# Kernel tuning notes

Hardware: AMD Instinct MI355X
Metric: run time of the kernel (lower is better)

The kernel has to match this reference:

```python
import jax, jax.numpy as jnp
import numpy as np


def setup_inputs() -> dict:
    key = jax.random.key(0)
    k1, k2, k3 = jax.random.split(key, 3)
    B, E, L, D = 32, 256, 2048, 256
    doc_state = jax.random.normal(k1, (B, L, D), dtype=jnp.float32)
    entity_mapping = jax.random.uniform(k2, (B, E, L), dtype=jnp.float32)
    entity_lens = jax.random.uniform(k3, (B, E), dtype=jnp.float32)
    return {"doc_state": doc_state, "entity_mapping": entity_mapping, "entity_lens": entity_lens}


def reference(doc_state, entity_mapping, entity_lens):
    # Original: (entity_mapping[:, :, :, None] * doc_state[:, None, :, :]).sum(2) / entity_lens[:, :, None]
    # This is a batched contraction over L; express as einsum to avoid the
    # huge [B, E, L, D] intermediate.
    summed = jnp.einsum('bel,bld->bed', entity_mapping, doc_state)  # [B, E, D]
    return summed / entity_lens[:, :, None]
```

## Files before the change

### kernel.cpp

```cpp
#include <hip/hip_runtime.h>
#include <stdint.h>

#define B_ 32
#define E_ 256
#define L_ 2048
#define D_ 256

#define BE 64
#define BD 128
#define BK 64
#define NKT (L_ / BK)

typedef __attribute__((ext_vector_type(4))) float  f32x4;
typedef __attribute__((ext_vector_type(4))) short  s16x4;
typedef __attribute__((ext_vector_type(8))) short  s16x8;

__device__ __forceinline__ void cvt_hilo4(const f32x4 v, s16x4 &h, s16x4 &l) {
    #pragma unroll
    for (int i = 0; i < 4; ++i) {
        unsigned u = __builtin_bit_cast(unsigned, (float)v[i]);
        h[i] = (short)(u >> 16);
        float hf = __builtin_bit_cast(float, u & 0xFFFF0000u);
        unsigned r = __builtin_bit_cast(unsigned, (float)(v[i] - hf));
        l[i] = (short)(r >> 16);
    }
}

__global__ __launch_bounds__(512, 2)
void mean_pool_kernel(const float* __restrict__ doc,
                      const float* __restrict__ emap,
                      const float* __restrict__ lens,
                      float* __restrict__ out) {
    __shared__ __align__(16) short As_hi[BE][BK];
    __shared__ __align__(16) short As_lo[BE][BK];
    __shared__ __align__(16) short Bs_hi[BD][BK];
    __shared__ __align__(16) short Bs_lo[BD][BK];
    __shared__ float lens_s[BE];

    const int t   = threadIdx.x;
    const int blk = blockIdx.x;
    const int b   = blk >> 3;
    const int e0  = ((blk >> 1) & 3) * BE;
    const int d0  = (blk & 1) * BD;

    const float* Ag = emap + ((size_t)b * E_ + e0) * L_;
    const float* Sg = doc  + (size_t)b * L_ * D_ + d0;

    if (t < BE) lens_s[t] = lens[b * E_ + e0 + t];

    const int a_c4 = t & 15;
    const int a_r  = t >> 4;
    const int s_db = t & 31;
    const int s_kb = t >> 5;

    const int lane = t & 63;
    const int w    = t >> 6;
    const int eo   = (w & 1) * 32;
    const int dq   = (w >> 1) * 32;
    const int ml   = lane & 15;
    const int kg   = lane >> 4;

    f32x4 acc[2][2] = {};
    f32x4 pa[2], pb[4];

    #pragma unroll
    for (int rr = 0; rr < 2; ++rr)
        pa[rr] = *(const f32x4*)(Ag + (size_t)(a_r + rr * 32) * L_ + a_c4 * 4);
    #pragma unroll
    for (int i = 0; i < 4; ++i)
        pb[i] = *(const f32x4*)(Sg + (size_t)(s_kb * 4 + i) * D_ + s_db * 4);

    for (int kt = 0; kt < NKT; ++kt) {
        #pragma unroll
        for (int rr = 0; rr < 2; ++rr) {
            const int row = a_r + rr * 32;
            s16x4 h, l;
            cvt_hilo4(pa[rr], h, l);
            const int col = (((a_c4 >> 1) ^ (row & 7)) << 3) + (a_c4 & 1) * 4;
            *(s16x4*)&As_hi[row][col] = h;
            *(s16x4*)&As_lo[row][col] = l;
        }
        #pragma unroll
        for (int dd = 0; dd < 4; ++dd) {
            const int row = s_db * 4 + dd;
            f32x4 tv = { pb[0][dd], pb[1][dd], pb[2][dd], pb[3][dd] };
            s16x4 h, l;
            cvt_hilo4(tv, h, l);
            const int col = (((s_kb >> 1) ^ (s_db & 7)) << 3) + (s_kb & 1) * 4;
            *(s16x4*)&Bs_hi[row][col] = h;
            *(s16x4*)&Bs_lo[row][col] = l;
        }
        __syncthreads();

        if (kt + 1 < NKT) {
            const int k0 = (kt + 1) * BK;
            #pragma unroll
            for (int rr = 0; rr < 2; ++rr)
                pa[rr] = *(const f32x4*)(Ag + (size_t)(a_r + rr * 32) * L_ + k0 + a_c4 * 4);
            #pragma unroll
            for (int i = 0; i < 4; ++i)
                pb[i] = *(const f32x4*)(Sg + (size_t)(k0 + s_kb * 4 + i) * D_ + s_db * 4);
        }

        #pragma unroll
        for (int kc = 0; kc < BK; kc += 32) {
            const int gbase = kc >> 3;
            s16x8 ah[2], al[2], bh[2], bl[2];
            #pragma unroll
            for (int mi = 0; mi < 2; ++mi) {
                const int row = eo + mi * 16 + ml;
                const int col = ((gbase + kg) ^ (row & 7)) << 3;
                ah[mi] = *(const s16x8*)&As_hi[row][col];
                al[mi] = *(const s16x8*)&As_lo[row][col];
            }
            #pragma unroll
            for (int ni = 0; ni < 2; ++ni) {
                const int row = dq + ni * 16 + ml;
                const int col = ((gbase + kg) ^ ((row >> 2) & 7)) << 3;
                bh[ni] = *(const s16x8*)&Bs_hi[row][col];
                bl[ni] = *(const s16x8*)&Bs_lo[row][col];
            }
            #pragma unroll
            for (int mi = 0; mi < 2; ++mi)
                #pragma unroll
                for (int ni = 0; ni < 2; ++ni) {
                    acc[mi][ni] = __builtin_amdgcn_mfma_f32_16x16x32_bf16(ah[mi], bh[ni], acc[mi][ni], 0, 0, 0);
                    acc[mi][ni] = __builtin_amdgcn_mfma_f32_16x16x32_bf16(ah[mi], bl[ni], acc[mi][ni], 0, 0, 0);
                    acc[mi][ni] = __builtin_amdgcn_mfma_f32_16x16x32_bf16(al[mi], bh[ni], acc[mi][ni], 0, 0, 0);
                }
        }
        __syncthreads();
    }

    #pragma unroll
    for (int mi = 0; mi < 2; ++mi) {
        #pragma unroll
        for (int rr = 0; rr < 4; ++rr) {
            const int er = eo + mi * 16 + kg * 4 + rr;
            const float lv = lens_s[er];
            #pragma unroll
            for (int ni = 0; ni < 2; ++ni) {
                out[((size_t)(b * E_ + e0 + er)) * D_ + d0 + dq + ni * 16 + ml] =
                    acc[mi][ni][rr] / lv;
            }
        }
    }
}

extern "C" void kernel_launch(void* const* d_in, const int* in_sizes, int n_in,
                              void* d_out, int out_size, void* d_ws, size_t ws_size,
                              hipStream_t stream) {
    const float* doc  = (const float*)d_in[0];
    const float* emap = (const float*)d_in[1];
    const float* lens = (const float*)d_in[2];
    float* out = (float*)d_out;

    dim3 grid(B_ * (E_ / BE) * (D_ / BD));
    dim3 block(512);
    hipLaunchKernelGGL(mean_pool_kernel, grid, block, 0, stream,
                       doc, emap, lens, out);
}
```

Measured before the change: 191.2 us.

## Split the L reduction four ways with atomic accumulation and a zero-init kernel

```diff
diff --git a/kernel.cpp b/kernel.cpp
--- a/kernel.cpp
+++ b/kernel.cpp
@@ -9,24 +9,32 @@
 #define BE 64
 #define BD 128
 #define BK 64
-#define NKT (L_ / BK)
+#define KS 4
+#define KCHUNK (L_ / KS)
+#define NKT (KCHUNK / BK)
 
+typedef __attribute__((ext_vector_type(2))) float  f32x2;
 typedef __attribute__((ext_vector_type(4))) float  f32x4;
 typedef __attribute__((ext_vector_type(4))) short  s16x4;
 typedef __attribute__((ext_vector_type(8))) short  s16x8;
 
+__device__ __forceinline__ void cvt_hilo1(float x, short &h, short &l) {
+    unsigned u = __builtin_bit_cast(unsigned, x);
+    h = (short)(u >> 16);
+    float hf = __builtin_bit_cast(float, u & 0xFFFF0000u);
+    unsigned r = __builtin_bit_cast(unsigned, x - hf);
+    l = (short)(r >> 16);
+}
 __device__ __forceinline__ void cvt_hilo4(const f32x4 v, s16x4 &h, s16x4 &l) {
     #pragma unroll
-    for (int i = 0; i < 4; ++i) {
-        unsigned u = __builtin_bit_cast(unsigned, (float)v[i]);
-        h[i] = (short)(u >> 16);
-        float hf = __builtin_bit_cast(float, u & 0xFFFF0000u);
-        unsigned r = __builtin_bit_cast(unsigned, (float)(v[i] - hf));
-        l[i] = (short)(r >> 16);
-    }
+    for (int i = 0; i < 4; ++i) { short hh, ll; cvt_hilo1(v[i], hh, ll); h[i] = hh; l[i] = ll; }
 }
 
-__global__ __launch_bounds__(512, 2)
+__global__ void zero_out_kernel(f32x4* __restrict__ out) {
+    out[(size_t)blockIdx.x * 256 + threadIdx.x] = f32x4{0.f, 0.f, 0.f, 0.f};
+}
+
+__global__ __launch_bounds__(512, 6)
 void mean_pool_kernel(const float* __restrict__ doc,
                       const float* __restrict__ emap,
                       const float* __restrict__ lens,
@@ -39,19 +47,20 @@
 
     const int t   = threadIdx.x;
     const int blk = blockIdx.x;
-    const int b   = blk >> 3;
-    const int e0  = ((blk >> 1) & 3) * BE;
-    const int d0  = (blk & 1) * BD;
+    const int ks  = blk & 3;
+    const int d0  = ((blk >> 2) & 1) * BD;
+    const int e0  = ((blk >> 3) & 3) * BE;
+    const int b   = blk >> 5;
 
-    const float* Ag = emap + ((size_t)b * E_ + e0) * L_;
-    const float* Sg = doc  + (size_t)b * L_ * D_ + d0;
+    const float* Ag = emap + ((size_t)b * E_ + e0) * L_ + ks * KCHUNK;
+    const float* Sg = doc  + (size_t)b * L_ * D_ + (size_t)ks * KCHUNK * D_ + d0;
 
     if (t < BE) lens_s[t] = lens[b * E_ + e0 + t];
 
     const int a_c4 = t & 15;
     const int a_r  = t >> 4;
-    const int s_db = t & 31;
-    const int s_kb = t >> 5;
+    const int db = t & 63;
+    const int kb = t >> 6;
 
     const int lane = t & 63;
     const int w    = t >> 6;
@@ -61,14 +70,15 @@
     const int kg   = lane >> 4;
 
     f32x4 acc[2][2] = {};
-    f32x4 pa[2], pb[4];
+    f32x4 pa[2];
+    f32x2 pb[8];
 
     #pragma unroll
     for (int rr = 0; rr < 2; ++rr)
         pa[rr] = *(const f32x4*)(Ag + (size_t)(a_r + rr * 32) * L_ + a_c4 * 4);
     #pragma unroll
-    for (int i = 0; i < 4; ++i)
-        pb[i] = *(const f32x4*)(Sg + (size_t)(s_kb * 4 + i) * D_ + s_db * 4);
+    for (int i = 0; i < 8; ++i)
+        pb[i] = *(const f32x2*)(Sg + (size_t)(kb * 8 + i) * D_ + db * 2);
 
     for (int kt = 0; kt < NKT; ++kt) {
         #pragma unroll
@@ -81,14 +91,18 @@
             *(s16x4*)&As_lo[row][col] = l;
         }
         #pragma unroll
-        for (int dd = 0; dd < 4; ++dd) {
-            const int row = s_db * 4 + dd;
-            f32x4 tv = { pb[0][dd], pb[1][dd], pb[2][dd], pb[3][dd] };
-            s16x4 h, l;
-            cvt_hilo4(tv, h, l);
-            const int col = (((s_kb >> 1) ^ (s_db & 7)) << 3) + (s_kb & 1) * 4;
-            *(s16x4*)&Bs_hi[row][col] = h;
-            *(s16x4*)&Bs_lo[row][col] = l;
+        for (int dd = 0; dd < 2; ++dd) {
+            const int row = db * 2 + dd;
+            s16x8 h, l;
+            #pragma unroll
+            for (int j = 0; j < 8; ++j) {
+                short hh, ll; cvt_hilo1(pb[j][dd], hh, ll);
+                h[j] = hh; l[j] = ll;
+            }
+            const int key = (db & 3) | (((db >> 2) & 1) << 2);
+            const int col = (kb ^ key) << 3;
+            *(s16x8*)&Bs_hi[row][col] = h;
+            *(s16x8*)&Bs_lo[row][col] = l;
         }
         __syncthreads();
 
@@ -98,13 +112,13 @@
             for (int rr = 0; rr < 2; ++rr)
                 pa[rr] = *(const f32x4*)(Ag + (size_t)(a_r + rr * 32) * L_ + k0 + a_c4 * 4);
             #pragma unroll
-            for (int i = 0; i < 4; ++i)
-                pb[i] = *(const f32x4*)(Sg + (size_t)(k0 + s_kb * 4 + i) * D_ + s_db * 4);
+            for (int i = 0; i < 8; ++i)
+                pb[i] = *(const f32x2*)(Sg + (size_t)(k0 + kb * 8 + i) * D_ + db * 2);
         }
 
         #pragma unroll
-        for (int kc = 0; kc < BK; kc += 32) {
-            const int gbase = kc >> 3;
+        for (int kc = 0; kc < 2; ++kc) {
+            const int gbase = kc * 4;
             s16x8 ah[2], al[2], bh[2], bl[2];
             #pragma unroll
             for (int mi = 0; mi < 2; ++mi) {
@@ -116,7 +130,8 @@
             #pragma unroll
             for (int ni = 0; ni < 2; ++ni) {
                 const int row = dq + ni * 16 + ml;
-                const int col = ((gbase + kg) ^ ((row >> 2) & 7)) << 3;
+                const int keyB = ((row >> 1) & 3) | (((row >> 3) & 1) << 2);
+                const int col  = ((gbase + kg) ^ keyB) << 3;
                 bh[ni] = *(const s16x8*)&Bs_hi[row][col];
                 bl[ni] = *(const s16x8*)&Bs_lo[row][col];
             }
@@ -140,8 +155,8 @@
             const float lv = lens_s[er];
             #pragma unroll
             for (int ni = 0; ni < 2; ++ni) {
-                out[((size_t)(b * E_ + e0 + er)) * D_ + d0 + dq + ni * 16 + ml] =
-                    acc[mi][ni][rr] / lv;
+                atomicAdd(&out[((size_t)(b * E_ + e0 + er)) * D_ + d0 + dq + ni * 16 + ml],
+                          acc[mi][ni][rr] / lv);
             }
         }
     }
@@ -155,7 +170,9 @@
     const float* lens = (const float*)d_in[2];
     float* out = (float*)d_out;
 
-    dim3 grid(B_ * (E_ / BE) * (D_ / BD));
+    zero_out_kernel<<<dim3(out_size / (4 * 256)), dim3(256), 0, stream>>>((f32x4*)out);
+
+    dim3 grid(B_ * (E_ / BE) * (D_ / BD) * KS);
     dim3 block(512);
     hipLaunchKernelGGL(mean_pool_kernel, grid, block, 0, stream,
                        doc, emap, lens, out);
```

New measurement: 173.2 us. 9.4% less time.
